# Kernel optimization log

Measured on AMD Instinct MI355X. Metric: run time of the kernel, lower is better.

Reference implementation:

```python
import jax, jax.numpy as jnp
import numpy as np

B, S, D_MODEL, H = 2, 2048, 1024, 16
D_K = D_MODEL // H
THETA = 10000.0


def setup_inputs() -> dict:
    key = jax.random.key(0)
    k1, k2, k3 = jax.random.split(key, 3)
    x = jax.random.normal(k1, (B, S, D_MODEL), dtype=jnp.float32)
    token_positions = jnp.tile(jnp.arange(S, dtype=jnp.int32), (B, 1))
    qkv_w = jax.random.normal(k2, (3 * D_MODEL, D_MODEL), dtype=jnp.float32) * (D_MODEL ** -0.5)
    out_w = jax.random.normal(k3, (D_MODEL, D_MODEL), dtype=jnp.float32) * (D_MODEL ** -0.5)
    return {"x": x, "token_positions": token_positions, "qkv_w": qkv_w, "out_w": out_w}


def _apply_rope(t, pos):
    # t: [B, H, S, d_k], pos: [B, S]
    half = D_K // 2
    inv_freq = THETA ** (-jnp.arange(0, half, dtype=jnp.float32) * 2.0 / D_K)  # [half]
    ang = pos.astype(jnp.float32)[:, None, :, None] * inv_freq  # [B,1,S,half]
    cos, sin = jnp.cos(ang), jnp.sin(ang)
    t1 = t[..., 0::2]
    t2 = t[..., 1::2]
    r1 = t1 * cos - t2 * sin
    r2 = t1 * sin + t2 * cos
    # interleave back: [..., half, 2] -> [..., d_k]
    return jnp.stack([r1, r2], axis=-1).reshape(t.shape)


def reference(x, token_positions, qkv_w, out_w):
    # fused QKV projection (no bias)
    qkv = jnp.einsum('bsd,ed->bse', x, qkv_w)  # [B,S,3*D_MODEL]
    qkv = qkv.reshape(B, S, 3, H, D_K)
    q = jnp.transpose(qkv[:, :, 0], (0, 2, 1, 3))  # [B,H,S,d_k]
    k = jnp.transpose(qkv[:, :, 1], (0, 2, 1, 3))
    v = jnp.transpose(qkv[:, :, 2], (0, 2, 1, 3))
    q = _apply_rope(q, token_positions)
    k = _apply_rope(k, token_positions)
    scores = jnp.einsum('bhqd,bhkd->bhqk', q, k) / jnp.sqrt(jnp.asarray(D_K, x.dtype))
    causal = jnp.tril(jnp.ones((S, S), dtype=bool))
    neg_inf = jnp.finfo(scores.dtype).min
    scores = jnp.where(causal, scores, neg_inf)
    attn = jax.nn.softmax(scores, axis=-1)
    out = jnp.einsum('bhqk,bhkd->bhqd', attn, v)  # [B,H,S,d_k]
    out = jnp.transpose(out, (0, 2, 1, 3)).reshape(B, S, D_MODEL)
    return jnp.einsum('bsd,ed->bse', out, out_w)
```

## Files before the change

### kernel.cpp

```cpp
#include <hip/hip_runtime.h>
#include <cstdint>

typedef unsigned short u16;
typedef unsigned int u32;
typedef __attribute__((ext_vector_type(8))) short short8;
typedef __attribute__((ext_vector_type(4))) float f32x4;

static constexpr int Bc = 2, Sc = 2048, DMc = 1024, Hc = 16, DKc = 64;
static constexpr int Mc = Bc * Sc;
static constexpr int BHSc = Bc * Hc * Sc;

#if __has_builtin(__builtin_amdgcn_exp2f)
#define EXP2F(x) __builtin_amdgcn_exp2f(x)
#else
#define EXP2F(x) exp2f(x)
#endif

__device__ __forceinline__ float b2f(u16 u) { return __uint_as_float((u32)u << 16); }
__device__ __forceinline__ u16 f2b(float f) {
  u32 x = __float_as_uint(f);
  return (u16)((x + 0x7fffu + ((x >> 16) & 1u)) >> 16);
}
__device__ __forceinline__ u32 cvtpk(float lo, float hi) {
  u32 r;
  asm("v_cvt_pk_bf16_f32 %0, %1, %2" : "=v"(r) : "v"(lo), "v"(hi));
  return r;
}

__global__ __launch_bounds__(256)
void cvt3_k(const float* __restrict__ x, const float* __restrict__ qw,
            const float* __restrict__ ow,
            u16* __restrict__ xb, u16* __restrict__ qwb, u16* __restrict__ owb)
{
  const int i = blockIdx.x * 256 + threadIdx.x;
  const float* src; u16* dst; int j;
  if (i < 524288)      { src = x;  dst = xb;  j = i; }
  else if (i < 917504) { src = qw; dst = qwb; j = i - 524288; }
  else                 { src = ow; dst = owb; j = i - 917504; }
  const float4 a = *(const float4*)(src + (size_t)j * 8);
  const float4 b = *(const float4*)(src + (size_t)j * 8 + 4);
  uint4 o;
  o.x = cvtpk(a.x, a.y);
  o.y = cvtpk(a.z, a.w);
  o.z = cvtpk(b.x, b.y);
  o.w = cvtpk(b.z, b.w);
  *(uint4*)(dst + (size_t)j * 8) = o;
}

template <typename OutT>
__global__ __launch_bounds__(256, 2)
void gemm_bt128(const u16* __restrict__ A, const u16* __restrict__ W,
                OutT* __restrict__ C, int M, int N, int K)
{
  __shared__ u16 As[128 * 32];
  __shared__ u16 Bs[128 * 32];
  const int t = threadIdx.x;
  const int w = t >> 6, l = t & 63;
  const int wr = w >> 1, wc = w & 1;
  const int l4 = l >> 4, l15 = l & 15;
  const int bm = blockIdx.x, bn = blockIdx.y;

  f32x4 acc[4][4] = {};

  const int rowA = bm * 128, rowB = bn * 128;
  const int sr = l >> 2, sk = (l & 3) * 8;

  for (int k0 = 0; k0 < K; k0 += 32) {
    __syncthreads();
#pragma unroll
    for (int i = 0; i < 2; ++i) {
      const int chunk = i * 4 + w;
      const u16* ga = A + (size_t)(rowA + chunk * 16 + sr) * K + k0 + sk;
      const u16* gb = W + (size_t)(rowB + chunk * 16 + sr) * K + k0 + sk;
      __builtin_amdgcn_global_load_lds((const __attribute__((address_space(1))) void*)ga,
                                       (__attribute__((address_space(3))) void*)(As + chunk * 512), 16, 0, 0);
      __builtin_amdgcn_global_load_lds((const __attribute__((address_space(1))) void*)gb,
                                       (__attribute__((address_space(3))) void*)(Bs + chunk * 512), 16, 0, 0);
    }
    __syncthreads();
    short8 af[4], bf[4];
#pragma unroll
    for (int m = 0; m < 4; ++m)
      af[m] = *(const short8*)(As + (wr * 64 + m * 16 + l15) * 32 + l4 * 8);
#pragma unroll
    for (int n = 0; n < 4; ++n)
      bf[n] = *(const short8*)(Bs + (wc * 64 + n * 16 + l15) * 32 + l4 * 8);
#pragma unroll
    for (int m = 0; m < 4; ++m)
#pragma unroll
      for (int n = 0; n < 4; ++n)
        acc[m][n] = __builtin_amdgcn_mfma_f32_16x16x32_bf16(af[m], bf[n], acc[m][n], 0, 0, 0);
  }

#pragma unroll
  for (int m = 0; m < 4; ++m) {
    const int r0 = rowA + wr * 64 + m * 16 + l4 * 4;
#pragma unroll
    for (int n = 0; n < 4; ++n) {
      const int c0 = rowB + wc * 64 + n * 16 + l15;
#pragma unroll
      for (int r = 0; r < 4; ++r) {
        const float v = acc[m][n][r];
        if constexpr (sizeof(OutT) == 2)
          C[(size_t)(r0 + r) * N + c0] = (OutT)f2b(v);
        else
          C[(size_t)(r0 + r) * N + c0] = (OutT)v;
      }
    }
  }
}

__global__ void rope_table_k(float2* __restrict__ tab)
{
  const int idx = blockIdx.x * 256 + threadIdx.x;
  const int p = idx >> 5, i = idx & 31;
  const float invf = powf(10000.0f, -(float)(2 * i) / 64.0f);
  const float ang = (float)p * invf;
  tab[idx] = make_float2(cosf(ang), sinf(ang));
}

__global__ __launch_bounds__(256)
void rope_reshape_k(const u16* __restrict__ qkv, const int* __restrict__ tokpos,
                    const float2* __restrict__ tab,
                    u16* __restrict__ Q, u16* __restrict__ K, u16* __restrict__ Vt)
{
  __shared__ u16 Vs[64][72];
  const int t = threadIdx.x;
  const int st = blockIdx.x, h = blockIdx.y, b = blockIdx.z;

  {
    const int sl = t >> 2, iq = t & 3;
    const int s = st * 64 + sl;
    const int p = tokpos[b * Sc + s];
    const size_t row = (size_t)(b * Sc + s) * 3 * DMc + h * DKc + iq * 16;
    const size_t orow = ((size_t)(b * Hc + h) * Sc + s) * DKc + iq * 16;
#pragma unroll
    for (int which = 0; which < 2; ++which) {
      const u16* g = qkv + row + which * DMc;
      uint4 va = *(const uint4*)g;
      uint4 vb = *(const uint4*)(g + 8);
      u32 in[8] = {va.x, va.y, va.z, va.w, vb.x, vb.y, vb.z, vb.w};
      const float scale = (which == 0) ? 0.18033688011112f : 1.0f;
      u32 ow[8];
#pragma unroll
      for (int j = 0; j < 8; ++j) {
        const float2 cs = tab[p * 32 + iq * 8 + j];
        const float t1 = b2f((u16)(in[j] & 0xffffu));
        const float t2 = b2f((u16)(in[j] >> 16));
        ow[j] = cvtpk((t1 * cs.x - t2 * cs.y) * scale, (t1 * cs.y + t2 * cs.x) * scale);
      }
      u16* dst = (which == 0 ? Q : K) + orow;
      *(uint4*)dst = make_uint4(ow[0], ow[1], ow[2], ow[3]);
      *(uint4*)(dst + 8) = make_uint4(ow[4], ow[5], ow[6], ow[7]);
    }
  }
#pragma unroll
  for (int it = 0; it < 2; ++it) {
    const int sv = it * 32 + (t >> 3);
    const int d0 = (t & 7) * 8;
    const u16* g = qkv + (size_t)(b * Sc + st * 64 + sv) * 3 * DMc + 2 * DMc + h * DKc + d0;
    *(uint4*)&Vs[sv][d0] = *(const uint4*)g;
  }
  __syncthreads();
  {
    const int d = t >> 2, s0 = (t & 3) * 16;
    u16 tmp[16];
#pragma unroll
    for (int j = 0; j < 16; ++j) tmp[j] = Vs[s0 + j][d];
    u16* dst = Vt + ((size_t)(b * Hc + h) * DKc + d) * Sc + st * 64 + s0;
    *(uint4*)dst = *(const uint4*)tmp;
    *(uint4*)(dst + 8) = *(const uint4*)(tmp + 8);
  }
}

__global__ __launch_bounds__(256, 4)
void attn_k(const u16* __restrict__ Q, const u16* __restrict__ K,
            const u16* __restrict__ Vt, u16* __restrict__ Opart,
            float2* __restrict__ ML)
{
  __shared__ u16 Kls[2][64 * 64];
  __shared__ u16 Vls[2][64 * 64];

  const int t = threadIdx.x, w = t >> 6, l = t & 63;
  const int l4 = l >> 4, l15 = l & 15;

  int bid = blockIdx.x;
  bid = (bid & 7) * 128 + (bid >> 3);
  const int p = bid & 15, part = (bid >> 4) & 1, h = (bid >> 5) & 15, b = bid >> 9;

  const int bh = b * Hc + h;
  const u16* Qb = Q + (size_t)bh * Sc * DKc;
  const u16* Kb = K + (size_t)bh * Sc * DKc;
  const u16* Vb = Vt + (size_t)bh * DKc * Sc;
  const int swz = (l15 & 7) << 4;

  const int qt0 = 31 - p, qt1 = p;
  const int q00 = qt0 * 64 + w * 16, q01 = qt1 * 64 + w * 16;
  const int n0 = (qt0 + 2 - part) >> 1, n1 = (qt1 + 2 - part) >> 1;
  const int ntot = n0 + n1;

  const short8 qf0a = *(const short8*)(Qb + (size_t)(q00 + l15) * DKc + l4 * 8);
  const short8 qf0b = *(const short8*)(Qb + (size_t)(q00 + l15) * DKc + 32 + l4 * 8);
  const short8 qf1a = *(const short8*)(Qb + (size_t)(q01 + l15) * DKc + l4 * 8);
  const short8 qf1b = *(const short8*)(Qb + (size_t)(q01 + l15) * DKc + 32 + l4 * 8);

  int srow[2], scol[2];
#pragma unroll
  for (int j = 0; j < 2; ++j) {
    const int e = j * 256 + t;
    srow[j] = e >> 3;
    scol[j] = (((e & 7) * 16) ^ ((srow[j] & 7) << 4)) >> 1;
  }
  auto stage = [&](int buf, int kv0) {
#pragma unroll
    for (int j = 0; j < 2; ++j) {
      const u16* gk = Kb + (size_t)(kv0 + srow[j]) * DKc + scol[j];
      __builtin_amdgcn_global_load_lds((const __attribute__((address_space(1))) void*)gk,
          (__attribute__((address_space(3))) void*)(&Kls[buf][0] + (j * 256 + w * 64) * 8), 16, 0, 0);
    }
#pragma unroll
    for (int j = 0; j < 2; ++j) {
      const u16* gv = Vb + (size_t)srow[j] * Sc + kv0 + scol[j];
      __builtin_amdgcn_global_load_lds((const __attribute__((address_space(1))) void*)gv,
          (__attribute__((address_space(3))) void*)(&Vls[buf][0] + (j * 256 + w * 64) * 8), 16, 0, 0);
    }
  };
  auto kvof = [&](int i) {
    return ((i < n0) ? (part + 2 * i) : (part + 2 * (i - n0))) * 64;
  };

  f32x4 o[4] = {};
  float m = -1e30f, lsum = 0.f;
  int qcur = q00;
  short8 qfA = qf0a, qfB = qf0b;

  auto epi = [&](int qbase) {
    const size_t pbase = ((size_t)part * Bc * Hc + bh) * Sc;
    if (l < 16) ML[pbase + qbase + l15] = make_float2(m, lsum);
#pragma unroll
    for (int dc = 0; dc < 4; ++dc)
#pragma unroll
      for (int r = 0; r < 4; ++r)
        Opart[(pbase + qbase + l4 * 4 + r) * 64 + dc * 16 + l15] =
            (u16)cvtpk(o[dc][r], o[dc][r]);
  };

  stage(0, kvof(0));
  for (int i = 0; i < ntot; ++i) {
    const int buf = i & 1;
    const int kv0 = kvof(i);
    asm volatile("s_waitcnt vmcnt(0)" ::: "memory");
    __builtin_amdgcn_s_barrier();
    if (i + 1 < ntot) stage(buf ^ 1, kvof(i + 1));

    const char* Kbuf = (const char*)&Kls[buf][0];
    const char* Vbuf = (const char*)&Vls[buf][0];
    char* Pw = (char*)&Kls[buf][0] + w * 2048;

    f32x4 sc[4];
    __builtin_amdgcn_s_setprio(1);
#pragma unroll
    for (int c = 0; c < 4; ++c) {
      const int rb = (c * 16 + l15) * 128;
      const short8 ka  = *(const short8*)(Kbuf + rb + ((l4 * 16) ^ swz));
      const short8 kb2 = *(const short8*)(Kbuf + rb + ((64 + l4 * 16) ^ swz));
      f32x4 z = {0.f, 0.f, 0.f, 0.f};
      z = __builtin_amdgcn_mfma_f32_16x16x32_bf16(ka, qfA, z, 0, 0, 0);
      z = __builtin_amdgcn_mfma_f32_16x16x32_bf16(kb2, qfB, z, 0, 0, 0);
      sc[c] = z;
    }
    __builtin_amdgcn_s_setprio(0);
    if (kv0 + 63 > qcur) {
#pragma unroll
      for (int c = 0; c < 4; ++c) {
        const int kvr = kv0 + c * 16 + l4 * 4;
#pragma unroll
        for (int r = 0; r < 4; ++r)
          if (kvr + r > qcur + l15) sc[c][r] = -1e30f;
      }
    }
    float pmax = -1e30f;
#pragma unroll
    for (int c = 0; c < 4; ++c)
      pmax = fmaxf(pmax, fmaxf(fmaxf(sc[c][0], sc[c][1]), fmaxf(sc[c][2], sc[c][3])));
    pmax = fmaxf(pmax, __shfl_xor(pmax, 16));
    pmax = fmaxf(pmax, __shfl_xor(pmax, 32));
    if (!__all(pmax - m <= 8.0f)) {
      const float mnew = fmaxf(m, pmax);
      const float fac = EXP2F(m - mnew);
      float f4[4];
#pragma unroll
      for (int r = 0; r < 4; ++r) f4[r] = __shfl(fac, l4 * 4 + r);
#pragma unroll
      for (int dc = 0; dc < 4; ++dc) {
        o[dc][0] *= f4[0]; o[dc][1] *= f4[1];
        o[dc][2] *= f4[2]; o[dc][3] *= f4[3];
      }
      lsum *= fac;
      m = mnew;
    }
    float rs = 0.f;
    u32 pk[4][2];
#pragma unroll
    for (int c = 0; c < 4; ++c) {
      const float p0 = EXP2F(sc[c][0] - m);
      const float p1 = EXP2F(sc[c][1] - m);
      const float p2 = EXP2F(sc[c][2] - m);
      const float p3 = EXP2F(sc[c][3] - m);
      rs += (p0 + p1) + (p2 + p3);
      pk[c][0] = cvtpk(p0, p1);
      pk[c][1] = cvtpk(p2, p3);
    }
    rs += __shfl_xor(rs, 16);
    rs += __shfl_xor(rs, 32);
    lsum += rs;

    asm volatile("s_waitcnt lgkmcnt(0)" ::: "memory");
    __builtin_amdgcn_s_barrier();

#pragma unroll
    for (int c = 0; c < 4; ++c) {
      uint2 u; u.x = pk[c][0]; u.y = pk[c][1];
      *(uint2*)(Pw + ((l15 * 128 + c * 32 + l4 * 8) ^ swz)) = u;
    }
    __builtin_amdgcn_s_setprio(1);
#pragma unroll
    for (int kv2 = 0; kv2 < 2; ++kv2) {
      const short8 pa = *(const short8*)(Pw + ((l15 * 128 + kv2 * 64 + l4 * 16) ^ swz));
#pragma unroll
      for (int dc = 0; dc < 4; ++dc) {
        const short8 vf = *(const short8*)(Vbuf + (dc * 16 + l15) * 128 + ((kv2 * 64 + l4 * 16) ^ swz));
        o[dc] = __builtin_amdgcn_mfma_f32_16x16x32_bf16(pa, vf, o[dc], 0, 0, 0);
      }
    }
    __builtin_amdgcn_s_setprio(0);

    if (i == n0 - 1) {
      epi(q00);
#pragma unroll
      for (int dc = 0; dc < 4; ++dc) o[dc] = f32x4{0.f, 0.f, 0.f, 0.f};
      m = -1e30f; lsum = 0.f;
      qcur = q01; qfA = qf1a; qfB = qf1b;
    }
  }
  epi(q01);
}

__global__ __launch_bounds__(256)
void combine_k(const u16* __restrict__ Opart, const float2* __restrict__ ML,
               u16* __restrict__ Oa)
{
  const int idx = blockIdx.x * 256 + threadIdx.x;
  const int row = idx >> 4, c4 = idx & 15;
  const float2 a = ML[row], bm2 = ML[BHSc + row];
  const float m = fmaxf(a.x, bm2.x);
  const float w0 = EXP2F(a.x - m), w1 = EXP2F(bm2.x - m);
  const float inv = 1.0f / (w0 * a.y + w1 * bm2.y);
  const uint2 u0 = *(const uint2*)(Opart + (size_t)row * 64 + c4 * 4);
  const uint2 u1 = *(const uint2*)(Opart + ((size_t)BHSc + row) * 64 + c4 * 4);
  const float r0 = (w0 * b2f((u16)u0.x) + w1 * b2f((u16)u1.x)) * inv;
  const float r1 = (w0 * b2f((u16)(u0.x >> 16)) + w1 * b2f((u16)(u1.x >> 16))) * inv;
  const float r2 = (w0 * b2f((u16)u0.y) + w1 * b2f((u16)u1.y)) * inv;
  const float r3 = (w0 * b2f((u16)(u0.y >> 16)) + w1 * b2f((u16)(u1.y >> 16))) * inv;
  const int s = row & (Sc - 1), bh = row >> 11, b = bh >> 4, h = bh & 15;
  uint2 pk;
  pk.x = cvtpk(r0, r1);
  pk.y = cvtpk(r2, r3);
  *(uint2*)(Oa + ((size_t)(b * Sc + s) * DMc + h * DKc + c4 * 4)) = pk;
}

extern "C" void kernel_launch(void* const* d_in, const int* in_sizes, int n_in,
                              void* d_out, int out_size, void* d_ws, size_t ws_size,
                              hipStream_t stream)
{
  const float* x      = (const float*)d_in[0];
  const int*   tokpos = (const int*)d_in[1];
  const float* qkv_w  = (const float*)d_in[2];
  const float* out_w  = (const float*)d_in[3];
  float* out = (float*)d_out;

  char* ws = (char*)d_ws;
  size_t off = 0;
  u16*   qkv   = (u16*)(ws + off);
  u16*   xb    = (u16*)(ws + off + 25165824);
  u16*   qwb   = (u16*)(ws + off + 33554432);
  u16*   Opart = (u16*)(ws + off);
  float2* ML   = (float2*)(ws + off + 33554432);
  off += 39845888;
  u16* owb = (u16*)(ws + off); off += (size_t)DMc * DMc * 2;
  u16* Qr  = (u16*)(ws + off); off += (size_t)BHSc * DKc * 2;
  u16* Kr  = (u16*)(ws + off); off += (size_t)BHSc * DKc * 2;
  u16* Vt  = (u16*)(ws + off); off += (size_t)BHSc * DKc * 2;
  u16* Oa  = (u16*)(ws + off); off += (size_t)Mc * DMc * 2;
  float2* tab = (float2*)(ws + off); off += (size_t)Sc * 32 * sizeof(float2);

  cvt3_k<<<4096, 256, 0, stream>>>(x, qkv_w, out_w, xb, qwb, owb);
  rope_table_k<<<(Sc * 32) / 256, 256, 0, stream>>>(tab);
  gemm_bt128<u16><<<dim3(Mc / 128, 3 * DMc / 128), 256, 0, stream>>>(xb, qwb, qkv, Mc, 3 * DMc, DMc);
  rope_reshape_k<<<dim3(Sc / 64, Hc, Bc), 256, 0, stream>>>(qkv, tokpos, tab, Qr, Kr, Vt);
  attn_k<<<1024, 256, 0, stream>>>(Qr, Kr, Vt, Opart, ML);
  combine_k<<<BHSc * 16 / 256, 256, 0, stream>>>(Opart, ML, Oa);
  gemm_bt128<float><<<dim3(Mc / 128, DMc / 128), 256, 0, stream>>>(Oa, owb, out, Mc, DMc, DMc);
}
```

Measured before the change: 123.5 us.

## Process 32 query rows per wave and split KV into four parts

Each wave now handles two 16-row query sub-tiles (128-row query tiles per block) and shares each K/V LDS fragment across both, doubling MFMA work per staged byte. The KV range is split into four interleaved parts instead of two, so the combine kernel now merges four partial results. V fragments are preloaded into registers and the P staging for the second sub-tile reuses the V LDS buffer. The cost is higher register pressure (occupancy hint lowered from 4 to 3), more partial-output traffic, and a heavier combine step.

```diff
diff --git a/kernel.cpp b/kernel.cpp
--- a/kernel.cpp
+++ b/kernel.cpp
@@ -173,7 +173,7 @@
   }
 }
 
-__global__ __launch_bounds__(256, 4)
+__global__ __launch_bounds__(256, 3)
 void attn_k(const u16* __restrict__ Q, const u16* __restrict__ K,
             const u16* __restrict__ Vt, u16* __restrict__ Opart,
             float2* __restrict__ ML)
@@ -186,7 +186,7 @@
 
   int bid = blockIdx.x;
   bid = (bid & 7) * 128 + (bid >> 3);
-  const int p = bid & 15, part = (bid >> 4) & 1, h = (bid >> 5) & 15, b = bid >> 9;
+  const int part = bid & 3, p = (bid >> 2) & 7, h = (bid >> 5) & 15, b = bid >> 9;
 
   const int bh = b * Hc + h;
   const u16* Qb = Q + (size_t)bh * Sc * DKc;
@@ -194,15 +194,11 @@
   const u16* Vb = Vt + (size_t)bh * DKc * Sc;
   const int swz = (l15 & 7) << 4;
 
-  const int qt0 = 31 - p, qt1 = p;
-  const int q00 = qt0 * 64 + w * 16, q01 = qt1 * 64 + w * 16;
-  const int n0 = (qt0 + 2 - part) >> 1, n1 = (qt1 + 2 - part) >> 1;
+  const int qt0 = 15 - p, qt1 = p;
+  const int q00 = qt0 * 128 + w * 32, q01 = qt1 * 128 + w * 32;
+  const int n0 = (2 * qt0 + 5 - part) >> 2;
+  const int n1 = (2 * qt1 + 5 - part) >> 2;
   const int ntot = n0 + n1;
-
-  const short8 qf0a = *(const short8*)(Qb + (size_t)(q00 + l15) * DKc + l4 * 8);
-  const short8 qf0b = *(const short8*)(Qb + (size_t)(q00 + l15) * DKc + 32 + l4 * 8);
-  const short8 qf1a = *(const short8*)(Qb + (size_t)(q01 + l15) * DKc + l4 * 8);
-  const short8 qf1b = *(const short8*)(Qb + (size_t)(q01 + l15) * DKc + 32 + l4 * 8);
 
   int srow[2], scol[2];
 #pragma unroll
@@ -226,23 +222,31 @@
     }
   };
   auto kvof = [&](int i) {
-    return ((i < n0) ? (part + 2 * i) : (part + 2 * (i - n0))) * 64;
+    return ((i < n0) ? (part + 4 * i) : (part + 4 * (i - n0))) * 64;
   };
 
-  f32x4 o[4] = {};
-  float m = -1e30f, lsum = 0.f;
+  short8 qA0 = *(const short8*)(Qb + (size_t)(q00 + l15) * DKc + l4 * 8);
+  short8 qA1 = *(const short8*)(Qb + (size_t)(q00 + l15) * DKc + 32 + l4 * 8);
+  short8 qB0 = *(const short8*)(Qb + (size_t)(q00 + 16 + l15) * DKc + l4 * 8);
+  short8 qB1 = *(const short8*)(Qb + (size_t)(q00 + 16 + l15) * DKc + 32 + l4 * 8);
+
+  f32x4 oA[4] = {}, oB[4] = {};
+  float mA = -1e20f, mB = -1e20f, lsA = 0.f, lsB = 0.f;
   int qcur = q00;
-  short8 qfA = qf0a, qfB = qf0b;
 
   auto epi = [&](int qbase) {
     const size_t pbase = ((size_t)part * Bc * Hc + bh) * Sc;
-    if (l < 16) ML[pbase + qbase + l15] = make_float2(m, lsum);
+    if (l < 16) ML[pbase + qbase + l15] = make_float2(mA, lsA);
+    else if (l < 32) ML[pbase + qbase + 16 + l15] = make_float2(mB, lsB);
 #pragma unroll
     for (int dc = 0; dc < 4; ++dc)
 #pragma unroll
-      for (int r = 0; r < 4; ++r)
+      for (int r = 0; r < 4; ++r) {
         Opart[(pbase + qbase + l4 * 4 + r) * 64 + dc * 16 + l15] =
-            (u16)cvtpk(o[dc][r], o[dc][r]);
+            (u16)cvtpk(oA[dc][r], oA[dc][r]);
+        Opart[(pbase + qbase + 16 + l4 * 4 + r) * 64 + dc * 16 + l15] =
+            (u16)cvtpk(oB[dc][r], oB[dc][r]);
+      }
   };
 
   stage(0, kvof(0));
@@ -255,82 +259,110 @@
 
     const char* Kbuf = (const char*)&Kls[buf][0];
     const char* Vbuf = (const char*)&Vls[buf][0];
-    char* Pw = (char*)&Kls[buf][0] + w * 2048;
-
-    f32x4 sc[4];
+    char* PwA = (char*)&Kls[buf][0] + w * 2048;
+    char* PwB = (char*)&Vls[buf][0] + w * 2048;
+
+    f32x4 scA[4], scB[4];
     __builtin_amdgcn_s_setprio(1);
 #pragma unroll
     for (int c = 0; c < 4; ++c) {
       const int rb = (c * 16 + l15) * 128;
       const short8 ka  = *(const short8*)(Kbuf + rb + ((l4 * 16) ^ swz));
       const short8 kb2 = *(const short8*)(Kbuf + rb + ((64 + l4 * 16) ^ swz));
-      f32x4 z = {0.f, 0.f, 0.f, 0.f};
-      z = __builtin_amdgcn_mfma_f32_16x16x32_bf16(ka, qfA, z, 0, 0, 0);
-      z = __builtin_amdgcn_mfma_f32_16x16x32_bf16(kb2, qfB, z, 0, 0, 0);
-      sc[c] = z;
+      f32x4 zA = {0.f, 0.f, 0.f, 0.f}, zB = {0.f, 0.f, 0.f, 0.f};
+      zA = __builtin_amdgcn_mfma_f32_16x16x32_bf16(ka, qA0, zA, 0, 0, 0);
+      zA = __builtin_amdgcn_mfma_f32_16x16x32_bf16(kb2, qA1, zA, 0, 0, 0);
+      zB = __builtin_amdgcn_mfma_f32_16x16x32_bf16(ka, qB0, zB, 0, 0, 0);
+      zB = __builtin_amdgcn_mfma_f32_16x16x32_bf16(kb2, qB1, zB, 0, 0, 0);
+      scA[c] = zA; scB[c] = zB;
     }
     __builtin_amdgcn_s_setprio(0);
+
+    short8 vf[2][4];
+#pragma unroll
+    for (int kv2 = 0; kv2 < 2; ++kv2)
+#pragma unroll
+      for (int dc = 0; dc < 4; ++dc)
+        vf[kv2][dc] = *(const short8*)(Vbuf + (dc * 16 + l15) * 128 + ((kv2 * 64 + l4 * 16) ^ swz));
+
     if (kv0 + 63 > qcur) {
 #pragma unroll
       for (int c = 0; c < 4; ++c) {
         const int kvr = kv0 + c * 16 + l4 * 4;
 #pragma unroll
         for (int r = 0; r < 4; ++r)
-          if (kvr + r > qcur + l15) sc[c][r] = -1e30f;
-      }
-    }
-    float pmax = -1e30f;
-#pragma unroll
-    for (int c = 0; c < 4; ++c)
-      pmax = fmaxf(pmax, fmaxf(fmaxf(sc[c][0], sc[c][1]), fmaxf(sc[c][2], sc[c][3])));
-    pmax = fmaxf(pmax, __shfl_xor(pmax, 16));
-    pmax = fmaxf(pmax, __shfl_xor(pmax, 32));
-    if (!__all(pmax - m <= 8.0f)) {
-      const float mnew = fmaxf(m, pmax);
-      const float fac = EXP2F(m - mnew);
-      float f4[4];
-#pragma unroll
-      for (int r = 0; r < 4; ++r) f4[r] = __shfl(fac, l4 * 4 + r);
-#pragma unroll
-      for (int dc = 0; dc < 4; ++dc) {
-        o[dc][0] *= f4[0]; o[dc][1] *= f4[1];
-        o[dc][2] *= f4[2]; o[dc][3] *= f4[3];
-      }
-      lsum *= fac;
-      m = mnew;
-    }
-    float rs = 0.f;
-    u32 pk[4][2];
+          if (kvr + r > qcur + l15) scA[c][r] = -1e30f;
+      }
+    }
+    if (kv0 + 63 > qcur + 16) {
+#pragma unroll
+      for (int c = 0; c < 4; ++c) {
+        const int kvr = kv0 + c * 16 + l4 * 4;
+#pragma unroll
+        for (int r = 0; r < 4; ++r)
+          if (kvr + r > qcur + 16 + l15) scB[c][r] = -1e30f;
+      }
+    }
+
+    float pmA = -1e30f, pmB = -1e30f;
 #pragma unroll
     for (int c = 0; c < 4; ++c) {
-      const float p0 = EXP2F(sc[c][0] - m);
-      const float p1 = EXP2F(sc[c][1] - m);
-      const float p2 = EXP2F(sc[c][2] - m);
-      const float p3 = EXP2F(sc[c][3] - m);
-      rs += (p0 + p1) + (p2 + p3);
-      pk[c][0] = cvtpk(p0, p1);
-      pk[c][1] = cvtpk(p2, p3);
-    }
-    rs += __shfl_xor(rs, 16);
-    rs += __shfl_xor(rs, 32);
-    lsum += rs;
+      pmA = fmaxf(pmA, fmaxf(fmaxf(scA[c][0], scA[c][1]), fmaxf(scA[c][2], scA[c][3])));
+      pmB = fmaxf(pmB, fmaxf(fmaxf(scB[c][0], scB[c][1]), fmaxf(scB[c][2], scB[c][3])));
+    }
+    pmA = fmaxf(pmA, __shfl_xor(pmA, 16)); pmA = fmaxf(pmA, __shfl_xor(pmA, 32));
+    pmB = fmaxf(pmB, __shfl_xor(pmB, 16)); pmB = fmaxf(pmB, __shfl_xor(pmB, 32));
+    if (!__all(fmaxf(pmA - mA, pmB - mB) <= 8.0f)) {
+      const float mnA = fmaxf(mA, pmA), mnB = fmaxf(mB, pmB);
+      const float fA = EXP2F(mA - mnA), fB = EXP2F(mB - mnB);
+      float f4A[4], f4B[4];
+#pragma unroll
+      for (int r = 0; r < 4; ++r) {
+        f4A[r] = __shfl(fA, l4 * 4 + r);
+        f4B[r] = __shfl(fB, l4 * 4 + r);
+      }
+#pragma unroll
+      for (int dc = 0; dc < 4; ++dc)
+#pragma unroll
+        for (int r = 0; r < 4; ++r) { oA[dc][r] *= f4A[r]; oB[dc][r] *= f4B[r]; }
+      lsA *= fA; lsB *= fB; mA = mnA; mB = mnB;
+    }
+    float rsA = 0.f, rsB = 0.f;
+    u32 pkA[4][2], pkB[4][2];
+#pragma unroll
+    for (int c = 0; c < 4; ++c) {
+      const float a0 = EXP2F(scA[c][0] - mA), a1 = EXP2F(scA[c][1] - mA);
+      const float a2 = EXP2F(scA[c][2] - mA), a3 = EXP2F(scA[c][3] - mA);
+      rsA += (a0 + a1) + (a2 + a3);
+      pkA[c][0] = cvtpk(a0, a1); pkA[c][1] = cvtpk(a2, a3);
+      const float b0 = EXP2F(scB[c][0] - mB), b1 = EXP2F(scB[c][1] - mB);
+      const float b2 = EXP2F(scB[c][2] - mB), b3 = EXP2F(scB[c][3] - mB);
+      rsB += (b0 + b1) + (b2 + b3);
+      pkB[c][0] = cvtpk(b0, b1); pkB[c][1] = cvtpk(b2, b3);
+    }
+    rsA += __shfl_xor(rsA, 16); rsA += __shfl_xor(rsA, 32);
+    rsB += __shfl_xor(rsB, 16); rsB += __shfl_xor(rsB, 32);
+    lsA += rsA; lsB += rsB;
 
     asm volatile("s_waitcnt lgkmcnt(0)" ::: "memory");
     __builtin_amdgcn_s_barrier();
 
 #pragma unroll
     for (int c = 0; c < 4; ++c) {
-      uint2 u; u.x = pk[c][0]; u.y = pk[c][1];
-      *(uint2*)(Pw + ((l15 * 128 + c * 32 + l4 * 8) ^ swz)) = u;
+      uint2 uA; uA.x = pkA[c][0]; uA.y = pkA[c][1];
+      *(uint2*)(PwA + ((l15 * 128 + c * 32 + l4 * 8) ^ swz)) = uA;
+      uint2 uB; uB.x = pkB[c][0]; uB.y = pkB[c][1];
+      *(uint2*)(PwB + ((l15 * 128 + c * 32 + l4 * 8) ^ swz)) = uB;
     }
     __builtin_amdgcn_s_setprio(1);
 #pragma unroll
     for (int kv2 = 0; kv2 < 2; ++kv2) {
-      const short8 pa = *(const short8*)(Pw + ((l15 * 128 + kv2 * 64 + l4 * 16) ^ swz));
+      const short8 paA = *(const short8*)(PwA + ((l15 * 128 + kv2 * 64 + l4 * 16) ^ swz));
+      const short8 paB = *(const short8*)(PwB + ((l15 * 128 + kv2 * 64 + l4 * 16) ^ swz));
 #pragma unroll
       for (int dc = 0; dc < 4; ++dc) {
-        const short8 vf = *(const short8*)(Vbuf + (dc * 16 + l15) * 128 + ((kv2 * 64 + l4 * 16) ^ swz));
-        o[dc] = __builtin_amdgcn_mfma_f32_16x16x32_bf16(pa, vf, o[dc], 0, 0, 0);
+        oA[dc] = __builtin_amdgcn_mfma_f32_16x16x32_bf16(paA, vf[kv2][dc], oA[dc], 0, 0, 0);
+        oB[dc] = __builtin_amdgcn_mfma_f32_16x16x32_bf16(paB, vf[kv2][dc], oB[dc], 0, 0, 0);
       }
     }
     __builtin_amdgcn_s_setprio(0);
@@ -338,9 +370,16 @@
     if (i == n0 - 1) {
       epi(q00);
 #pragma unroll
-      for (int dc = 0; dc < 4; ++dc) o[dc] = f32x4{0.f, 0.f, 0.f, 0.f};
-      m = -1e30f; lsum = 0.f;
-      qcur = q01; qfA = qf1a; qfB = qf1b;
+      for (int dc = 0; dc < 4; ++dc) {
+        oA[dc] = f32x4{0.f, 0.f, 0.f, 0.f};
+        oB[dc] = f32x4{0.f, 0.f, 0.f, 0.f};
+      }
+      mA = mB = -1e20f; lsA = lsB = 0.f;
+      qcur = q01;
+      qA0 = *(const short8*)(Qb + (size_t)(q01 + l15) * DKc + l4 * 8);
+      qA1 = *(const short8*)(Qb + (size_t)(q01 + l15) * DKc + 32 + l4 * 8);
+      qB0 = *(const short8*)(Qb + (size_t)(q01 + 16 + l15) * DKc + l4 * 8);
+      qB1 = *(const short8*)(Qb + (size_t)(q01 + 16 + l15) * DKc + 32 + l4 * 8);
     }
   }
   epi(q01);
@@ -352,20 +391,28 @@
 {
   const int idx = blockIdx.x * 256 + threadIdx.x;
   const int row = idx >> 4, c4 = idx & 15;
-  const float2 a = ML[row], bm2 = ML[BHSc + row];
-  const float m = fmaxf(a.x, bm2.x);
-  const float w0 = EXP2F(a.x - m), w1 = EXP2F(bm2.x - m);
-  const float inv = 1.0f / (w0 * a.y + w1 * bm2.y);
-  const uint2 u0 = *(const uint2*)(Opart + (size_t)row * 64 + c4 * 4);
-  const uint2 u1 = *(const uint2*)(Opart + ((size_t)BHSc + row) * 64 + c4 * 4);
-  const float r0 = (w0 * b2f((u16)u0.x) + w1 * b2f((u16)u1.x)) * inv;
-  const float r1 = (w0 * b2f((u16)(u0.x >> 16)) + w1 * b2f((u16)(u1.x >> 16))) * inv;
-  const float r2 = (w0 * b2f((u16)u0.y) + w1 * b2f((u16)u1.y)) * inv;
-  const float r3 = (w0 * b2f((u16)(u0.y >> 16)) + w1 * b2f((u16)(u1.y >> 16))) * inv;
+  float2 ml[4];
+#pragma unroll
+  for (int q = 0; q < 4; ++q) ml[q] = ML[(size_t)q * BHSc + row];
+  const float m = fmaxf(fmaxf(ml[0].x, ml[1].x), fmaxf(ml[2].x, ml[3].x));
+  float wgt[4];
+  float den = 0.f;
+#pragma unroll
+  for (int q = 0; q < 4; ++q) { wgt[q] = EXP2F(ml[q].x - m); den += wgt[q] * ml[q].y; }
+  const float inv = 1.0f / den;
+  float r0 = 0.f, r1 = 0.f, r2 = 0.f, r3 = 0.f;
+#pragma unroll
+  for (int q = 0; q < 4; ++q) {
+    const uint2 u = *(const uint2*)(Opart + ((size_t)q * BHSc + row) * 64 + c4 * 4);
+    r0 += wgt[q] * b2f((u16)u.x);
+    r1 += wgt[q] * b2f((u16)(u.x >> 16));
+    r2 += wgt[q] * b2f((u16)u.y);
+    r3 += wgt[q] * b2f((u16)(u.y >> 16));
+  }
   const int s = row & (Sc - 1), bh = row >> 11, b = bh >> 4, h = bh & 15;
   uint2 pk;
-  pk.x = cvtpk(r0, r1);
-  pk.y = cvtpk(r2, r3);
+  pk.x = cvtpk(r0 * inv, r1 * inv);
+  pk.y = cvtpk(r2 * inv, r3 * inv);
   *(uint2*)(Oa + ((size_t)(b * Sc + s) * DMc + h * DKc + c4 * 4)) = pk;
 }
 
```

Result: slower. 153.5 us (+24.2%).
